# Optimization experiments

Measured on AMD Instinct MI355X. Metric: run time of the kernel, lower is better.

Reference implementation:

```python
import jax, jax.numpy as jnp
import numpy as np

D_MODEL = 1024
NUM_HEADS = 16
OUT_SHAPE = (64,)            # ControlGate `shape`; d_head = prod(OUT_SHAPE)
BANK_SIZE = 16
TOP_K = 2
BATCH, SEQ = 8, 4096
D_OUT = NUM_HEADS * int(np.prod(OUT_SHAPE))  # 1024


def setup_inputs() -> dict:
    key = jax.random.key(0)
    k1, k2, k3, k4 = jax.random.split(key, 4)
    tensor = jax.random.normal(k1, (BATCH, SEQ, D_MODEL), dtype=jnp.float32)
    sel_idx = jax.random.randint(k2, (BATCH, TOP_K), 0, BANK_SIZE)
    sel_probs = jax.random.uniform(k3, (BATCH, TOP_K), dtype=jnp.float32)
    sel_probs = sel_probs / jnp.sum(sel_probs, axis=-1, keepdims=True)
    W = jax.random.normal(k4, (BANK_SIZE, D_MODEL, D_OUT), dtype=jnp.float32) * 0.02
    b = jnp.zeros((BANK_SIZE, D_OUT), dtype=jnp.float32)
    return {"tensor": tensor, "sel_idx": sel_idx, "sel_probs": sel_probs, "W": W, "b": b}


def reference(tensor, sel_idx, sel_probs, W, b):
    # --- VirtualMakeHeads: bank-selected (virtual) linear projection ---
    # Superimpose the selected weight banks per batch element.
    W_sel = W[sel_idx]                    # (B, K, d_model, d_out)  irregular gather
    b_sel = b[sel_idx]                    # (B, K, d_out)
    W_eff = jnp.einsum('bk,bkio->bio', sel_probs, W_sel)   # (B, d_model, d_out)
    b_eff = jnp.einsum('bk,bko->bo', sel_probs, b_sel)     # (B, d_out)
    logits = jnp.einsum('bsi,bio->bso', tensor, W_eff) + b_eff[:, None, :]
    # reshape to heads: (B, S, num_heads, d_head)
    logits = logits.reshape(*logits.shape[:-1], NUM_HEADS, -1)
    # --- ControlGate: unflatten last dim into OUT_SHAPE ---
    logits = logits.reshape(*logits.shape[:-1], *OUT_SHAPE)
    # DropoutLogits with p=0.0 (eval) is identity.
    # activation == 'sigmoid'
    return jax.nn.sigmoid(logits)
```

## Files before the change

### kernel.cpp

```cpp
#include <hip/hip_runtime.h>
#include <hip/hip_bf16.h>

#define B_  8
#define S_  4096
#define DM  1024
#define DO  1024

typedef __attribute__((ext_vector_type(4))) float f32x4;
typedef __attribute__((ext_vector_type(8))) short bf16x8;

__device__ inline unsigned int pkbf(float a, float b) {
    __hip_bfloat162 h = __float22bfloat162_rn(float2{a, b});
    union { __hip_bfloat162 h2; unsigned int u; } cv;
    cv.h2 = h;
    return cv.u;
}

__global__ __launch_bounds__(256) void prep_wpack(
    const float* __restrict__ W, const int* __restrict__ sel_idx,
    const float* __restrict__ sel_probs, unsigned short* __restrict__ wpack)
{
    const int kt = blockIdx.x, nb = blockIdx.y, b = blockIdx.z;
    const int i0 = sel_idx[b*2+0], i1 = sel_idx[b*2+1];
    const float p0 = sel_probs[b*2+0], p1 = sel_probs[b*2+1];
    const int t = threadIdx.x;
    const int col = t & 127;
    const int gh  = t >> 7;

    const int o = nb * 128 + col;
    const float* w0 = W + (size_t)i0 * DM * DO + (size_t)(kt * 32) * DO + o;
    const float* w1 = W + (size_t)i1 * DM * DO + (size_t)(kt * 32) * DO + o;

    char* tile = (char*)wpack + ((size_t)((b * 8 + nb) * 32 + kt)) * 8192;
    const int q = (col >> 1) & 3;

    #pragma unroll
    for (int gg = 0; gg < 2; ++gg) {
        const int g = gh * 2 + gg;
        float v[8];
        #pragma unroll
        for (int j = 0; j < 8; ++j)
            v[j] = p0 * w0[(size_t)(g * 8 + j) * DO] + p1 * w1[(size_t)(g * 8 + j) * DO];
        uint4 u;
        u.x = pkbf(v[0], v[1]); u.y = pkbf(v[2], v[3]);
        u.z = pkbf(v[4], v[5]); u.w = pkbf(v[6], v[7]);
        *reinterpret_cast<uint4*>(tile + col * 64 + ((g ^ q) << 4)) = u;
    }
}

__global__ __launch_bounds__(256) void prep_beff(
    const float* __restrict__ bias, const int* __restrict__ sel_idx,
    const float* __restrict__ sel_probs, float* __restrict__ beff)
{
    const int b = blockIdx.x;
    const int i0 = sel_idx[b*2+0], i1 = sel_idx[b*2+1];
    const float p0 = sel_probs[b*2+0], p1 = sel_probs[b*2+1];
    for (int o = threadIdx.x; o < DO; o += blockDim.x)
        beff[(size_t)b * DO + o] = p0 * bias[(size_t)i0 * DO + o]
                                 + p1 * bias[(size_t)i1 * DO + o];
}

__global__ __launch_bounds__(256, 4) void gemm4(
    const float* __restrict__ X, const unsigned short* __restrict__ wpack,
    const float* __restrict__ beff, float* __restrict__ out)
{
    __shared__ char lds[32768];

    const int id = blockIdx.x;
    const int swz = (id & 7) * 256 + (id >> 3);
    const int b  = swz >> 8;
    const int bm = (swz >> 3) & 31;
    const int nb = swz & 7;

    const int t = threadIdx.x;
    const int wave = t >> 6, lane = t & 63;
    const int wm = wave >> 1, wn = wave & 1;
    const int fr = lane & 15, fq = lane >> 4;

    const int s_row = t >> 1;
    const int s_h   = t & 1;
    const float* xrow = X + ((size_t)(b * S_ + bm * 128 + s_row)) * DM + s_h * 16;
    const int sq = (s_row >> 1) & 3;
    const int wrA0 = s_row * 64 + (((s_h * 2 + 0) ^ sq) << 4);
    const int wrA1 = s_row * 64 + (((s_h * 2 + 1) ^ sq) << 4);

    const char* wtile = (const char*)wpack + ((size_t)((b * 8 + nb) * 32)) * 8192;

    const int axor = (fr >> 1) & 3;
    const int rdA = (wm * 64 + fr) * 64 + ((fq ^ axor) << 4);
    const int rdB = (wn * 64 + fr) * 64 + ((fq ^ axor) << 4);

    f32x4 acc[4][4] = {};
    float4 ax0, ax1, ax2, ax3;

#define LOAD_X(KT)                                                            \
    {   const float* s = xrow + (KT) * 32;                                    \
        ax0 = *reinterpret_cast<const float4*>(s);                            \
        ax1 = *reinterpret_cast<const float4*>(s + 4);                        \
        ax2 = *reinterpret_cast<const float4*>(s + 8);                        \
        ax3 = *reinterpret_cast<const float4*>(s + 12); }

#define STAGE_B(KT, BOFF)                                                     \
    {   const char* gB = wtile + (size_t)(KT) * 8192;                         \
        _Pragma("unroll")                                                     \
        for (int r = 0; r < 2; ++r)                                           \
            __builtin_amdgcn_global_load_lds(                                 \
                (const __attribute__((address_space(1))) void*)(gB + (wave*2+r)*1024 + lane*16), \
                (__attribute__((address_space(3))) void*)(lds + (BOFF) + (wave*2+r)*1024),       \
                16, 0, 0); }

#define WRITE_A(AOFF)                                                         \
    {   uint4 u0, u1;                                                         \
        u0.x = pkbf(ax0.x, ax0.y); u0.y = pkbf(ax0.z, ax0.w);                 \
        u0.z = pkbf(ax1.x, ax1.y); u0.w = pkbf(ax1.z, ax1.w);                 \
        u1.x = pkbf(ax2.x, ax2.y); u1.y = pkbf(ax2.z, ax2.w);                 \
        u1.z = pkbf(ax3.x, ax3.y); u1.w = pkbf(ax3.z, ax3.w);                 \
        *reinterpret_cast<uint4*>(lds + (AOFF) + wrA0) = u0;                  \
        *reinterpret_cast<uint4*>(lds + (AOFF) + wrA1) = u1; }

    LOAD_X(0);
    __builtin_amdgcn_sched_barrier(0);
    STAGE_B(0, 16384);
    __builtin_amdgcn_sched_barrier(0);
    WRITE_A(0);
    __syncthreads();

    for (int kt = 0; kt < 32; ++kt) {
        const int cur = (kt & 1) * 8192;
        const int nxt = 8192 - cur;

        if (kt < 31) {
            LOAD_X(kt + 1);
            __builtin_amdgcn_sched_barrier(0);
            STAGE_B(kt + 1, 16384 + nxt);
            __builtin_amdgcn_sched_barrier(0);
        }

        bf16x8 bf[4];
        #pragma unroll
        for (int nf = 0; nf < 4; ++nf)
            bf[nf] = *reinterpret_cast<const bf16x8*>(lds + 16384 + cur + rdB + nf * 1024);
        #pragma unroll
        for (int m = 0; m < 4; ++m) {
            bf16x8 af = *reinterpret_cast<const bf16x8*>(lds + cur + rdA + m * 1024);
            #pragma unroll
            for (int nf = 0; nf < 4; ++nf)
                acc[m][nf] = __builtin_amdgcn_mfma_f32_16x16x32_bf16(af, bf[nf], acc[m][nf], 0, 0, 0);
        }

        if (kt < 31) { WRITE_A(nxt); }
        __syncthreads();
    }

    const float* be = beff + (size_t)b * DO + nb * 128 + wn * 64;
    float bv[4];
    #pragma unroll
    for (int nf = 0; nf < 4; ++nf) bv[nf] = be[nf * 16 + fr];

    float* ob = out + ((size_t)(b * S_ + bm * 128 + wm * 64)) * DO + nb * 128 + wn * 64;
    #pragma unroll
    for (int m = 0; m < 4; ++m) {
        #pragma unroll
        for (int nf = 0; nf < 4; ++nf) {
            const int col = nf * 16 + fr;
            #pragma unroll
            for (int r = 0; r < 4; ++r) {
                const int row = m * 16 + fq * 4 + r;
                const float xv = acc[m][nf][r] + bv[nf];
                ob[(size_t)row * DO + col] = 1.0f / (1.0f + __expf(-xv));
            }
        }
    }
#undef LOAD_X
#undef STAGE_B
#undef WRITE_A
}

extern "C" void kernel_launch(void* const* d_in, const int* in_sizes, int n_in,
                              void* d_out, int out_size, void* d_ws, size_t ws_size,
                              hipStream_t stream) {
    const float* tensor    = (const float*)d_in[0];
    const int*   sel_idx   = (const int*)d_in[1];
    const float* sel_probs = (const float*)d_in[2];
    const float* W         = (const float*)d_in[3];
    const float* bias      = (const float*)d_in[4];
    float* out = (float*)d_out;

    unsigned short* wpack = (unsigned short*)d_ws;
    float* beff = (float*)((char*)d_ws + (size_t)8 * 8 * 32 * 8192);

    hipLaunchKernelGGL(prep_wpack, dim3(32, 8, 8), dim3(256), 0, stream,
                       W, sel_idx, sel_probs, wpack);
    hipLaunchKernelGGL(prep_beff, dim3(8), dim3(256), 0, stream,
                       bias, sel_idx, sel_probs, beff);
    hipLaunchKernelGGL(gemm4, dim3(2048), dim3(256), 0, stream,
                       tensor, wpack, beff, out);
}
```

Measured before the change: 165.5 us.

## Pre-pack X to bf16 and use larger 256x256 GEMM tiles with async LDS loads

```diff
diff --git a/kernel.cpp b/kernel.cpp
--- a/kernel.cpp
+++ b/kernel.cpp
@@ -16,7 +16,204 @@
     return cv.u;
 }
 
-__global__ __launch_bounds__(256) void prep_wpack(
+
+__global__ __launch_bounds__(256) void prep_xpack(
+    const float* __restrict__ X, unsigned short* __restrict__ xpack)
+{
+    const int kt = blockIdx.x, bm = blockIdx.y, b = blockIdx.z;
+    const int r = threadIdx.x;
+    const float* src = X + ((size_t)(b * S_ + bm * 256 + r)) * DM + kt * 64;
+    char* dst = (char*)xpack + ((size_t)((b * 16 + bm) * 16 + kt)) * 32768 + r * 128;
+    const int rx = r & 7;
+    #pragma unroll
+    for (int g = 0; g < 8; ++g) {
+        float4 a = *reinterpret_cast<const float4*>(src + g * 8);
+        float4 c = *reinterpret_cast<const float4*>(src + g * 8 + 4);
+        uint4 u;
+        u.x = pkbf(a.x, a.y); u.y = pkbf(a.z, a.w);
+        u.z = pkbf(c.x, c.y); u.w = pkbf(c.z, c.w);
+        *reinterpret_cast<uint4*>(dst + ((g ^ rx) << 4)) = u;
+    }
+}
+
+__global__ __launch_bounds__(256) void prep_wpack64(
+    const float* __restrict__ W, const int* __restrict__ sel_idx,
+    const float* __restrict__ sel_probs, unsigned short* __restrict__ wpack)
+{
+    const int kt = blockIdx.x, nb = blockIdx.y, b = blockIdx.z;
+    const int i0 = sel_idx[b*2+0], i1 = sel_idx[b*2+1];
+    const float p0 = sel_probs[b*2+0], p1 = sel_probs[b*2+1];
+    const int c = threadIdx.x;
+    const int o = nb * 256 + c;
+    const float* w0 = W + (size_t)i0 * DM * DO + (size_t)(kt * 64) * DO + o;
+    const float* w1 = W + (size_t)i1 * DM * DO + (size_t)(kt * 64) * DO + o;
+    char* dst = (char*)wpack + ((size_t)((b * 4 + nb) * 16 + kt)) * 32768 + c * 128;
+    const int cx = c & 7;
+    #pragma unroll
+    for (int g = 0; g < 8; ++g) {
+        float v[8];
+        #pragma unroll
+        for (int j = 0; j < 8; ++j)
+            v[j] = p0 * w0[(size_t)(g * 8 + j) * DO] + p1 * w1[(size_t)(g * 8 + j) * DO];
+        uint4 u;
+        u.x = pkbf(v[0], v[1]); u.y = pkbf(v[2], v[3]);
+        u.z = pkbf(v[4], v[5]); u.w = pkbf(v[6], v[7]);
+        *reinterpret_cast<uint4*>(dst + ((g ^ cx) << 4)) = u;
+    }
+}
+
+__global__ __launch_bounds__(256) void prep_beff(
+    const float* __restrict__ bias, const int* __restrict__ sel_idx,
+    const float* __restrict__ sel_probs, float* __restrict__ beff)
+{
+    const int b = blockIdx.x;
+    const int i0 = sel_idx[b*2+0], i1 = sel_idx[b*2+1];
+    const float p0 = sel_probs[b*2+0], p1 = sel_probs[b*2+1];
+    for (int o = threadIdx.x; o < DO; o += blockDim.x)
+        beff[(size_t)b * DO + o] = p0 * bias[(size_t)i0 * DO + o]
+                                 + p1 * bias[(size_t)i1 * DO + o];
+}
+
+__global__ __launch_bounds__(512, 2) void gemmx(
+    const unsigned short* __restrict__ xpack, const unsigned short* __restrict__ wpack,
+    const float* __restrict__ beff, float* __restrict__ out)
+{
+    extern __shared__ char lds[];
+
+    const int id = blockIdx.x;
+    const int swz = (id & 7) * 64 + (id >> 3);
+    const int b  = swz >> 6;
+    const int bm = (swz >> 2) & 15;
+    const int nb = swz & 3;
+
+    const int t = threadIdx.x;
+    const int wave = t >> 6, lane = t & 63;
+    const int wm = wave >> 2, wnw = wave & 3;
+    const int fr = lane & 15, fq = lane >> 4;
+
+    const char* xt = (const char*)xpack + ((size_t)((b * 16 + bm) * 16)) * 32768;
+    const char* wt = (const char*)wpack + ((size_t)((b * 4 + nb) * 16)) * 32768;
+
+    const int s0 = ((fq ^ (fr & 7)) << 4);
+    const int s1 = (((4 + fq) ^ (fr & 7)) << 4);
+    const int rdA = wm * 16384 + fr * 128;
+    const int rdB = wnw * 8192 + fr * 128;
+
+    f32x4 acc[8][4] = {};
+
+#define GLOAD(SRC, DSTOFF, I)                                                 \
+    __builtin_amdgcn_global_load_lds(                                         \
+        (const __attribute__((address_space(1))) void*)((SRC) + wave*4096 + (I)*1024 + lane*16), \
+        (__attribute__((address_space(3))) void*)(lds + (DSTOFF) + wave*4096 + (I)*1024), 16, 0, 0)
+
+#define MFMA16(MB, AF, BK)                                                    \
+    __builtin_amdgcn_s_setprio(1);                                            \
+    _Pragma("unroll")                                                         \
+    for (int m = 0; m < 4; ++m) {                                             \
+        _Pragma("unroll")                                                     \
+        for (int nf = 0; nf < 4; ++nf)                                        \
+            acc[(MB)+m][nf] = __builtin_amdgcn_mfma_f32_16x16x32_bf16(        \
+                AF[m], BK[nf], acc[(MB)+m][nf], 0, 0, 0);                     \
+    }                                                                         \
+    __builtin_amdgcn_s_setprio(0);
+
+    #pragma unroll
+    for (int i = 0; i < 4; ++i) { GLOAD(xt, 0, i); GLOAD(wt, 65536, i); }
+    asm volatile("s_waitcnt vmcnt(0)" ::: "memory");
+    __builtin_amdgcn_s_barrier();
+
+    #pragma unroll 1
+    for (int kt = 0; kt < 16; ++kt) {
+        const int ca = (kt & 1) * 32768;
+        const int cb = 65536 + ca;
+        const int na = 32768 - ca;
+        const int nbf = 65536 + na;
+        const char* gxn = xt + (size_t)(kt + 1) * 32768;
+        const char* gwn = wt + (size_t)(kt + 1) * 32768;
+
+        bf16x8 bk[4], af[4];
+
+        #pragma unroll
+        for (int nf = 0; nf < 4; ++nf)
+            bk[nf] = *reinterpret_cast<const bf16x8*>(lds + cb + rdB + nf*2048 + s0);
+        #pragma unroll
+        for (int m = 0; m < 4; ++m)
+            af[m] = *reinterpret_cast<const bf16x8*>(lds + ca + rdA + m*2048 + s0);
+        __builtin_amdgcn_sched_barrier(0);
+        if (kt < 15) {
+            #pragma unroll
+            for (int i = 0; i < 4; ++i) { GLOAD(gxn, na, i); GLOAD(gwn, nbf, i); }
+        }
+        __builtin_amdgcn_sched_barrier(0);
+        __builtin_amdgcn_s_barrier();
+        asm volatile("s_waitcnt lgkmcnt(0)" ::: "memory");
+        __builtin_amdgcn_sched_barrier(0);
+        MFMA16(0, af, bk)
+        __builtin_amdgcn_sched_barrier(0);
+        __builtin_amdgcn_s_barrier();
+
+        #pragma unroll
+        for (int m = 0; m < 4; ++m)
+            af[m] = *reinterpret_cast<const bf16x8*>(lds + ca + rdA + (4+m)*2048 + s0);
+        __builtin_amdgcn_sched_barrier(0);
+        __builtin_amdgcn_s_barrier();
+        asm volatile("s_waitcnt lgkmcnt(0)" ::: "memory");
+        __builtin_amdgcn_sched_barrier(0);
+        MFMA16(4, af, bk)
+        __builtin_amdgcn_sched_barrier(0);
+        __builtin_amdgcn_s_barrier();
+
+        #pragma unroll
+        for (int nf = 0; nf < 4; ++nf)
+            bk[nf] = *reinterpret_cast<const bf16x8*>(lds + cb + rdB + nf*2048 + s1);
+        #pragma unroll
+        for (int m = 0; m < 4; ++m)
+            af[m] = *reinterpret_cast<const bf16x8*>(lds + ca + rdA + m*2048 + s1);
+        __builtin_amdgcn_sched_barrier(0);
+        __builtin_amdgcn_s_barrier();
+        asm volatile("s_waitcnt lgkmcnt(0)" ::: "memory");
+        __builtin_amdgcn_sched_barrier(0);
+        MFMA16(0, af, bk)
+        __builtin_amdgcn_sched_barrier(0);
+        __builtin_amdgcn_s_barrier();
+
+        #pragma unroll
+        for (int m = 0; m < 4; ++m)
+            af[m] = *reinterpret_cast<const bf16x8*>(lds + ca + rdA + (4+m)*2048 + s1);
+        __builtin_amdgcn_sched_barrier(0);
+        __builtin_amdgcn_s_barrier();
+        asm volatile("s_waitcnt lgkmcnt(0)" ::: "memory");
+        __builtin_amdgcn_sched_barrier(0);
+        MFMA16(4, af, bk)
+        __builtin_amdgcn_sched_barrier(0);
+        if (kt < 15) { asm volatile("s_waitcnt vmcnt(0)" ::: "memory"); }
+        __builtin_amdgcn_s_barrier();
+    }
+
+    const float* be = beff + (size_t)b * DO + nb * 256 + wnw * 64;
+    float bv[4];
+    #pragma unroll
+    for (int nf = 0; nf < 4; ++nf) bv[nf] = be[nf * 16 + fr];
+
+    float* ob = out + ((size_t)(b * S_ + bm * 256 + wm * 128)) * DO + nb * 256 + wnw * 64;
+    #pragma unroll
+    for (int mf = 0; mf < 8; ++mf) {
+        #pragma unroll
+        for (int nf = 0; nf < 4; ++nf) {
+            const int col = nf * 16 + fr;
+            #pragma unroll
+            for (int r = 0; r < 4; ++r) {
+                const int row = mf * 16 + fq * 4 + r;
+                const float xv = acc[mf][nf][r] + bv[nf];
+                ob[(size_t)row * DO + col] = 1.0f / (1.0f + __expf(-xv));
+            }
+        }
+    }
+#undef GLOAD
+#undef MFMA16
+}
+
+__global__ __launch_bounds__(256) void prep_wpack_f(
     const float* __restrict__ W, const int* __restrict__ sel_idx,
     const float* __restrict__ sel_probs, unsigned short* __restrict__ wpack)
 {
@@ -26,14 +223,11 @@
     const int t = threadIdx.x;
     const int col = t & 127;
     const int gh  = t >> 7;
-
     const int o = nb * 128 + col;
     const float* w0 = W + (size_t)i0 * DM * DO + (size_t)(kt * 32) * DO + o;
     const float* w1 = W + (size_t)i1 * DM * DO + (size_t)(kt * 32) * DO + o;
-
     char* tile = (char*)wpack + ((size_t)((b * 8 + nb) * 32 + kt)) * 8192;
     const int q = (col >> 1) & 3;
-
     #pragma unroll
     for (int gg = 0; gg < 2; ++gg) {
         const int g = gh * 2 + gg;
@@ -48,58 +242,38 @@
     }
 }
 
-__global__ __launch_bounds__(256) void prep_beff(
-    const float* __restrict__ bias, const int* __restrict__ sel_idx,
-    const float* __restrict__ sel_probs, float* __restrict__ beff)
-{
-    const int b = blockIdx.x;
-    const int i0 = sel_idx[b*2+0], i1 = sel_idx[b*2+1];
-    const float p0 = sel_probs[b*2+0], p1 = sel_probs[b*2+1];
-    for (int o = threadIdx.x; o < DO; o += blockDim.x)
-        beff[(size_t)b * DO + o] = p0 * bias[(size_t)i0 * DO + o]
-                                 + p1 * bias[(size_t)i1 * DO + o];
-}
-
 __global__ __launch_bounds__(256, 4) void gemm4(
     const float* __restrict__ X, const unsigned short* __restrict__ wpack,
     const float* __restrict__ beff, float* __restrict__ out)
 {
     __shared__ char lds[32768];
-
     const int id = blockIdx.x;
     const int swz = (id & 7) * 256 + (id >> 3);
     const int b  = swz >> 8;
     const int bm = (swz >> 3) & 31;
     const int nb = swz & 7;
-
     const int t = threadIdx.x;
     const int wave = t >> 6, lane = t & 63;
     const int wm = wave >> 1, wn = wave & 1;
     const int fr = lane & 15, fq = lane >> 4;
-
     const int s_row = t >> 1;
     const int s_h   = t & 1;
     const float* xrow = X + ((size_t)(b * S_ + bm * 128 + s_row)) * DM + s_h * 16;
     const int sq = (s_row >> 1) & 3;
     const int wrA0 = s_row * 64 + (((s_h * 2 + 0) ^ sq) << 4);
     const int wrA1 = s_row * 64 + (((s_h * 2 + 1) ^ sq) << 4);
-
     const char* wtile = (const char*)wpack + ((size_t)((b * 8 + nb) * 32)) * 8192;
-
     const int axor = (fr >> 1) & 3;
     const int rdA = (wm * 64 + fr) * 64 + ((fq ^ axor) << 4);
     const int rdB = (wn * 64 + fr) * 64 + ((fq ^ axor) << 4);
-
     f32x4 acc[4][4] = {};
     float4 ax0, ax1, ax2, ax3;
-
 #define LOAD_X(KT)                                                            \
     {   const float* s = xrow + (KT) * 32;                                    \
         ax0 = *reinterpret_cast<const float4*>(s);                            \
         ax1 = *reinterpret_cast<const float4*>(s + 4);                        \
         ax2 = *reinterpret_cast<const float4*>(s + 8);                        \
         ax3 = *reinterpret_cast<const float4*>(s + 12); }
-
 #define STAGE_B(KT, BOFF)                                                     \
     {   const char* gB = wtile + (size_t)(KT) * 8192;                         \
         _Pragma("unroll")                                                     \
@@ -108,7 +282,6 @@
                 (const __attribute__((address_space(1))) void*)(gB + (wave*2+r)*1024 + lane*16), \
                 (__attribute__((address_space(3))) void*)(lds + (BOFF) + (wave*2+r)*1024),       \
                 16, 0, 0); }
-
 #define WRITE_A(AOFF)                                                         \
     {   uint4 u0, u1;                                                         \
         u0.x = pkbf(ax0.x, ax0.y); u0.y = pkbf(ax0.z, ax0.w);                 \
@@ -117,25 +290,21 @@
         u1.z = pkbf(ax3.x, ax3.y); u1.w = pkbf(ax3.z, ax3.w);                 \
         *reinterpret_cast<uint4*>(lds + (AOFF) + wrA0) = u0;                  \
         *reinterpret_cast<uint4*>(lds + (AOFF) + wrA1) = u1; }
-
     LOAD_X(0);
     __builtin_amdgcn_sched_barrier(0);
     STAGE_B(0, 16384);
     __builtin_amdgcn_sched_barrier(0);
     WRITE_A(0);
     __syncthreads();
-
     for (int kt = 0; kt < 32; ++kt) {
         const int cur = (kt & 1) * 8192;
         const int nxt = 8192 - cur;
-
         if (kt < 31) {
             LOAD_X(kt + 1);
             __builtin_amdgcn_sched_barrier(0);
             STAGE_B(kt + 1, 16384 + nxt);
             __builtin_amdgcn_sched_barrier(0);
         }
-
         bf16x8 bf[4];
         #pragma unroll
         for (int nf = 0; nf < 4; ++nf)
@@ -147,16 +316,13 @@
             for (int nf = 0; nf < 4; ++nf)
                 acc[m][nf] = __builtin_amdgcn_mfma_f32_16x16x32_bf16(af, bf[nf], acc[m][nf], 0, 0, 0);
         }
-
         if (kt < 31) { WRITE_A(nxt); }
         __syncthreads();
     }
-
     const float* be = beff + (size_t)b * DO + nb * 128 + wn * 64;
     float bv[4];
     #pragma unroll
     for (int nf = 0; nf < 4; ++nf) bv[nf] = be[nf * 16 + fr];
-
     float* ob = out + ((size_t)(b * S_ + bm * 128 + wm * 64)) * DO + nb * 128 + wn * 64;
     #pragma unroll
     for (int m = 0; m < 4; ++m) {
@@ -186,13 +352,34 @@
     const float* bias      = (const float*)d_in[4];
     float* out = (float*)d_out;
 
-    unsigned short* wpack = (unsigned short*)d_ws;
-    float* beff = (float*)((char*)d_ws + (size_t)8 * 8 * 32 * 8192);
-
-    hipLaunchKernelGGL(prep_wpack, dim3(32, 8, 8), dim3(256), 0, stream,
-                       W, sel_idx, sel_probs, wpack);
-    hipLaunchKernelGGL(prep_beff, dim3(8), dim3(256), 0, stream,
-                       bias, sel_idx, sel_probs, beff);
-    hipLaunchKernelGGL(gemm4, dim3(2048), dim3(256), 0, stream,
-                       tensor, wpack, beff, out);
-}
+    const size_t XP = (size_t)2048 * 32768;
+    const size_t WP = (size_t)512 * 32768;
+    const size_t NEED = XP + WP + (size_t)B_ * DO * 4;
+
+    if (ws_size >= NEED) {
+        unsigned short* xpack = (unsigned short*)d_ws;
+        unsigned short* wpack = (unsigned short*)((char*)d_ws + XP);
+        float* beff = (float*)((char*)d_ws + XP + WP);
+
+        hipFuncSetAttribute((const void*)gemmx,
+                            hipFuncAttributeMaxDynamicSharedMemorySize, 131072);
+
+        hipLaunchKernelGGL(prep_xpack, dim3(16, 16, 8), dim3(256), 0, stream,
+                           tensor, xpack);
+        hipLaunchKernelGGL(prep_wpack64, dim3(16, 4, 8), dim3(256), 0, stream,
+                           W, sel_idx, sel_probs, wpack);
+        hipLaunchKernelGGL(prep_beff, dim3(8), dim3(256), 0, stream,
+                           bias, sel_idx, sel_probs, beff);
+        hipLaunchKernelGGL(gemmx, dim3(512), dim3(512), 131072, stream,
+                           xpack, wpack, beff, out);
+    } else {
+        unsigned short* wpack = (unsigned short*)d_ws;
+        float* beff = (float*)((char*)d_ws + (size_t)8 * 8 * 32 * 8192);
+        hipLaunchKernelGGL(prep_wpack_f, dim3(32, 8, 8), dim3(256), 0, stream,
+                           W, sel_idx, sel_probs, wpack);
+        hipLaunchKernelGGL(prep_beff, dim3(8), dim3(256), 0, stream,
+                           bias, sel_idx, sel_probs, beff);
+        hipLaunchKernelGGL(gemm4, dim3(2048), dim3(256), 0, stream,
+                           tensor, wpack, beff, out);
+    }
+}
```

After: 157.9 us. 4.6% less time.

## Pre-pack activations to swizzled bf16 tiles and stage both GEMM operands via direct LDS loads

Applied to the files above, without the earlier changes.

```diff
diff --git a/kernel.cpp b/kernel.cpp
--- a/kernel.cpp
+++ b/kernel.cpp
@@ -16,24 +16,169 @@
     return cv.u;
 }
 
+
+__global__ __launch_bounds__(256) void prep_xpack(
+    const float* __restrict__ X, unsigned short* __restrict__ xpack)
+{
+    const int bm = blockIdx.y, b = blockIdx.z;
+    const int t = threadIdx.x;
+    const int r  = t & 127;
+    const int kt = blockIdx.x * 2 + (t >> 7);
+    const float* src = X + ((size_t)(b * S_ + bm * 128 + r)) * DM + kt * 32;
+    char* dst = (char*)xpack + ((size_t)((b * 32 + bm) * 32 + kt)) * 8192 + r * 64;
+    const int q = (r >> 1) & 3;
+    #pragma unroll
+    for (int g = 0; g < 4; ++g) {
+        float4 a = *reinterpret_cast<const float4*>(src + g * 8);
+        float4 c = *reinterpret_cast<const float4*>(src + g * 8 + 4);
+        uint4 u;
+        u.x = pkbf(a.x, a.y); u.y = pkbf(a.z, a.w);
+        u.z = pkbf(c.x, c.y); u.w = pkbf(c.z, c.w);
+        *reinterpret_cast<uint4*>(dst + ((g ^ q) << 4)) = u;
+    }
+}
+
 __global__ __launch_bounds__(256) void prep_wpack(
     const float* __restrict__ W, const int* __restrict__ sel_idx,
     const float* __restrict__ sel_probs, unsigned short* __restrict__ wpack)
 {
+    const int nb = blockIdx.y, b = blockIdx.z;
+    const int i0 = sel_idx[b*2+0], i1 = sel_idx[b*2+1];
+    const float p0 = sel_probs[b*2+0], p1 = sel_probs[b*2+1];
+    const int t = threadIdx.x;
+    const int c  = t & 127;
+    const int kt = blockIdx.x * 2 + (t >> 7);
+    const int o = nb * 128 + c;
+    const float* w0 = W + (size_t)i0 * DM * DO + (size_t)(kt * 32) * DO + o;
+    const float* w1 = W + (size_t)i1 * DM * DO + (size_t)(kt * 32) * DO + o;
+    char* dst = (char*)wpack + ((size_t)((b * 8 + nb) * 32 + kt)) * 8192 + c * 64;
+    const int q = (c >> 1) & 3;
+    #pragma unroll
+    for (int g = 0; g < 4; ++g) {
+        float v[8];
+        #pragma unroll
+        for (int j = 0; j < 8; ++j)
+            v[j] = p0 * w0[(size_t)(g * 8 + j) * DO] + p1 * w1[(size_t)(g * 8 + j) * DO];
+        uint4 u;
+        u.x = pkbf(v[0], v[1]); u.y = pkbf(v[2], v[3]);
+        u.z = pkbf(v[4], v[5]); u.w = pkbf(v[6], v[7]);
+        *reinterpret_cast<uint4*>(dst + ((g ^ q) << 4)) = u;
+    }
+}
+
+__global__ __launch_bounds__(256) void prep_beff(
+    const float* __restrict__ bias, const int* __restrict__ sel_idx,
+    const float* __restrict__ sel_probs, float* __restrict__ beff)
+{
+    const int b = blockIdx.x;
+    const int i0 = sel_idx[b*2+0], i1 = sel_idx[b*2+1];
+    const float p0 = sel_probs[b*2+0], p1 = sel_probs[b*2+1];
+    for (int o = threadIdx.x; o < DO; o += blockDim.x)
+        beff[(size_t)b * DO + o] = p0 * bias[(size_t)i0 * DO + o]
+                                 + p1 * bias[(size_t)i1 * DO + o];
+}
+
+__global__ __launch_bounds__(256, 4) void gemm128(
+    const unsigned short* __restrict__ xpack, const unsigned short* __restrict__ wpack,
+    const float* __restrict__ beff, float* __restrict__ out)
+{
+    __shared__ char lds[32768];
+
+    const int id = blockIdx.x;
+    const int swz = (id & 7) * 256 + (id >> 3);
+    const int b  = swz >> 8;
+    const int bm = (swz >> 3) & 31;
+    const int nb = swz & 7;
+
+    const int t = threadIdx.x;
+    const int wave = t >> 6, lane = t & 63;
+    const int wm = wave >> 1, wn = wave & 1;
+    const int fr = lane & 15, fq = lane >> 4;
+
+    const char* xt = (const char*)xpack + ((size_t)((b * 32 + bm) * 32)) * 8192;
+    const char* wt = (const char*)wpack + ((size_t)((b * 8 + nb) * 32)) * 8192;
+
+    const int q   = (fr >> 1) & 3;
+    const int rdA = (wm * 64 + fr) * 64 + ((fq ^ q) << 4);
+    const int rdB = (wn * 64 + fr) * 64 + ((fq ^ q) << 4);
+
+    f32x4 acc[4][4] = {};
+
+#define GLOAD(SRC, DST)                                                        \
+    __builtin_amdgcn_global_load_lds(                                          \
+        (const __attribute__((address_space(1))) void*)(SRC),                  \
+        (__attribute__((address_space(3))) void*)(DST), 16, 0, 0)
+
+#define STAGE(KT, OFF)                                                         \
+    {   const char* ga = xt + (size_t)(KT) * 8192 + wave * 2048 + lane * 16;   \
+        const char* gb = wt + (size_t)(KT) * 8192 + wave * 2048 + lane * 16;   \
+        char* la = lds + (OFF) + wave * 2048;                                  \
+        char* lb = lds + 16384 + (OFF) + wave * 2048;                          \
+        GLOAD(ga, la); GLOAD(ga + 1024, la + 1024);                            \
+        GLOAD(gb, lb); GLOAD(gb + 1024, lb + 1024); }
+
+    STAGE(0, 0);
+    __syncthreads();
+
+    for (int kt = 0; kt < 32; ++kt) {
+        const int cur = (kt & 1) * 8192;
+        const int nxt = 8192 - cur;
+
+        if (kt < 31) { STAGE(kt + 1, nxt); }
+
+        bf16x8 bk[4];
+        #pragma unroll
+        for (int nf = 0; nf < 4; ++nf)
+            bk[nf] = *reinterpret_cast<const bf16x8*>(lds + 16384 + cur + rdB + nf * 1024);
+        #pragma unroll
+        for (int m = 0; m < 4; ++m) {
+            bf16x8 af = *reinterpret_cast<const bf16x8*>(lds + cur + rdA + m * 1024);
+            #pragma unroll
+            for (int nf = 0; nf < 4; ++nf)
+                acc[m][nf] = __builtin_amdgcn_mfma_f32_16x16x32_bf16(af, bk[nf], acc[m][nf], 0, 0, 0);
+        }
+
+        __syncthreads();
+    }
+
+    const float* be = beff + (size_t)b * DO + nb * 128 + wn * 64;
+    float bv[4];
+    #pragma unroll
+    for (int nf = 0; nf < 4; ++nf) bv[nf] = be[nf * 16 + fr];
+
+    float* ob = out + ((size_t)(b * S_ + bm * 128 + wm * 64)) * DO + nb * 128 + wn * 64;
+    #pragma unroll
+    for (int m = 0; m < 4; ++m) {
+        #pragma unroll
+        for (int nf = 0; nf < 4; ++nf) {
+            const int col = nf * 16 + fr;
+            #pragma unroll
+            for (int r = 0; r < 4; ++r) {
+                const int row = m * 16 + fq * 4 + r;
+                const float xv = acc[m][nf][r] + bv[nf];
+                ob[(size_t)row * DO + col] = 1.0f / (1.0f + __expf(-xv));
+            }
+        }
+    }
+#undef GLOAD
+#undef STAGE
+}
+
+__global__ __launch_bounds__(256) void prep_wpack_f(
+    const float* __restrict__ W, const int* __restrict__ sel_idx,
+    const float* __restrict__ sel_probs, unsigned short* __restrict__ wpack)
+{
     const int kt = blockIdx.x, nb = blockIdx.y, b = blockIdx.z;
     const int i0 = sel_idx[b*2+0], i1 = sel_idx[b*2+1];
     const float p0 = sel_probs[b*2+0], p1 = sel_probs[b*2+1];
     const int t = threadIdx.x;
     const int col = t & 127;
     const int gh  = t >> 7;
-
     const int o = nb * 128 + col;
     const float* w0 = W + (size_t)i0 * DM * DO + (size_t)(kt * 32) * DO + o;
     const float* w1 = W + (size_t)i1 * DM * DO + (size_t)(kt * 32) * DO + o;
-
     char* tile = (char*)wpack + ((size_t)((b * 8 + nb) * 32 + kt)) * 8192;
     const int q = (col >> 1) & 3;
-
     #pragma unroll
     for (int gg = 0; gg < 2; ++gg) {
         const int g = gh * 2 + gg;
@@ -48,58 +193,38 @@
     }
 }
 
-__global__ __launch_bounds__(256) void prep_beff(
-    const float* __restrict__ bias, const int* __restrict__ sel_idx,
-    const float* __restrict__ sel_probs, float* __restrict__ beff)
-{
-    const int b = blockIdx.x;
-    const int i0 = sel_idx[b*2+0], i1 = sel_idx[b*2+1];
-    const float p0 = sel_probs[b*2+0], p1 = sel_probs[b*2+1];
-    for (int o = threadIdx.x; o < DO; o += blockDim.x)
-        beff[(size_t)b * DO + o] = p0 * bias[(size_t)i0 * DO + o]
-                                 + p1 * bias[(size_t)i1 * DO + o];
-}
-
 __global__ __launch_bounds__(256, 4) void gemm4(
     const float* __restrict__ X, const unsigned short* __restrict__ wpack,
     const float* __restrict__ beff, float* __restrict__ out)
 {
     __shared__ char lds[32768];
-
     const int id = blockIdx.x;
     const int swz = (id & 7) * 256 + (id >> 3);
     const int b  = swz >> 8;
     const int bm = (swz >> 3) & 31;
     const int nb = swz & 7;
-
     const int t = threadIdx.x;
     const int wave = t >> 6, lane = t & 63;
     const int wm = wave >> 1, wn = wave & 1;
     const int fr = lane & 15, fq = lane >> 4;
-
     const int s_row = t >> 1;
     const int s_h   = t & 1;
     const float* xrow = X + ((size_t)(b * S_ + bm * 128 + s_row)) * DM + s_h * 16;
     const int sq = (s_row >> 1) & 3;
     const int wrA0 = s_row * 64 + (((s_h * 2 + 0) ^ sq) << 4);
     const int wrA1 = s_row * 64 + (((s_h * 2 + 1) ^ sq) << 4);
-
     const char* wtile = (const char*)wpack + ((size_t)((b * 8 + nb) * 32)) * 8192;
-
     const int axor = (fr >> 1) & 3;
     const int rdA = (wm * 64 + fr) * 64 + ((fq ^ axor) << 4);
     const int rdB = (wn * 64 + fr) * 64 + ((fq ^ axor) << 4);
-
     f32x4 acc[4][4] = {};
     float4 ax0, ax1, ax2, ax3;
-
 #define LOAD_X(KT)                                                            \
     {   const float* s = xrow + (KT) * 32;                                    \
         ax0 = *reinterpret_cast<const float4*>(s);                            \
         ax1 = *reinterpret_cast<const float4*>(s + 4);                        \
         ax2 = *reinterpret_cast<const float4*>(s + 8);                        \
         ax3 = *reinterpret_cast<const float4*>(s + 12); }
-
 #define STAGE_B(KT, BOFF)                                                     \
     {   const char* gB = wtile + (size_t)(KT) * 8192;                         \
         _Pragma("unroll")                                                     \
@@ -108,7 +233,6 @@
                 (const __attribute__((address_space(1))) void*)(gB + (wave*2+r)*1024 + lane*16), \
                 (__attribute__((address_space(3))) void*)(lds + (BOFF) + (wave*2+r)*1024),       \
                 16, 0, 0); }
-
 #define WRITE_A(AOFF)                                                         \
     {   uint4 u0, u1;                                                         \
         u0.x = pkbf(ax0.x, ax0.y); u0.y = pkbf(ax0.z, ax0.w);                 \
@@ -117,25 +241,21 @@
         u1.z = pkbf(ax3.x, ax3.y); u1.w = pkbf(ax3.z, ax3.w);                 \
         *reinterpret_cast<uint4*>(lds + (AOFF) + wrA0) = u0;                  \
         *reinterpret_cast<uint4*>(lds + (AOFF) + wrA1) = u1; }
-
     LOAD_X(0);
     __builtin_amdgcn_sched_barrier(0);
     STAGE_B(0, 16384);
     __builtin_amdgcn_sched_barrier(0);
     WRITE_A(0);
     __syncthreads();
-
     for (int kt = 0; kt < 32; ++kt) {
         const int cur = (kt & 1) * 8192;
         const int nxt = 8192 - cur;
-
         if (kt < 31) {
             LOAD_X(kt + 1);
             __builtin_amdgcn_sched_barrier(0);
             STAGE_B(kt + 1, 16384 + nxt);
             __builtin_amdgcn_sched_barrier(0);
         }
-
         bf16x8 bf[4];
         #pragma unroll
         for (int nf = 0; nf < 4; ++nf)
@@ -147,16 +267,13 @@
             for (int nf = 0; nf < 4; ++nf)
                 acc[m][nf] = __builtin_amdgcn_mfma_f32_16x16x32_bf16(af, bf[nf], acc[m][nf], 0, 0, 0);
         }
-
         if (kt < 31) { WRITE_A(nxt); }
         __syncthreads();
     }
-
     const float* be = beff + (size_t)b * DO + nb * 128 + wn * 64;
     float bv[4];
     #pragma unroll
     for (int nf = 0; nf < 4; ++nf) bv[nf] = be[nf * 16 + fr];
-
     float* ob = out + ((size_t)(b * S_ + bm * 128 + wm * 64)) * DO + nb * 128 + wn * 64;
     #pragma unroll
     for (int m = 0; m < 4; ++m) {
@@ -186,13 +303,31 @@
     const float* bias      = (const float*)d_in[4];
     float* out = (float*)d_out;
 
-    unsigned short* wpack = (unsigned short*)d_ws;
-    float* beff = (float*)((char*)d_ws + (size_t)8 * 8 * 32 * 8192);
-
-    hipLaunchKernelGGL(prep_wpack, dim3(32, 8, 8), dim3(256), 0, stream,
-                       W, sel_idx, sel_probs, wpack);
-    hipLaunchKernelGGL(prep_beff, dim3(8), dim3(256), 0, stream,
-                       bias, sel_idx, sel_probs, beff);
-    hipLaunchKernelGGL(gemm4, dim3(2048), dim3(256), 0, stream,
-                       tensor, wpack, beff, out);
-}
+    const size_t XP = (size_t)8192 * 8192;
+    const size_t WP = (size_t)2048 * 8192;
+    const size_t NEED = XP + WP + (size_t)B_ * DO * 4;
+
+    if (ws_size >= NEED) {
+        unsigned short* xpack = (unsigned short*)d_ws;
+        unsigned short* wpack = (unsigned short*)((char*)d_ws + XP);
+        float* beff = (float*)((char*)d_ws + XP + WP);
+
+        hipLaunchKernelGGL(prep_xpack, dim3(16, 32, 8), dim3(256), 0, stream,
+                           tensor, xpack);
+        hipLaunchKernelGGL(prep_wpack, dim3(16, 8, 8), dim3(256), 0, stream,
+                           W, sel_idx, sel_probs, wpack);
+        hipLaunchKernelGGL(prep_beff, dim3(8), dim3(256), 0, stream,
+                           bias, sel_idx, sel_probs, beff);
+        hipLaunchKernelGGL(gemm128, dim3(2048), dim3(256), 0, stream,
+                           xpack, wpack, beff, out);
+    } else {
+        unsigned short* wpack = (unsigned short*)d_ws;
+        float* beff = (float*)((char*)d_ws + (size_t)8 * 8 * 32 * 8192);
+        hipLaunchKernelGGL(prep_wpack_f, dim3(32, 8, 8), dim3(256), 0, stream,
+                           W, sel_idx, sel_probs, wpack);
+        hipLaunchKernelGGL(prep_beff, dim3(8), dim3(256), 0, stream,
+                           bias, sel_idx, sel_probs, beff);
+        hipLaunchKernelGGL(gemm4, dim3(2048), dim3(256), 0, stream,
+                           tensor, wpack, beff, out);
+    }
+}
```

Result: faster. 146.7 us (-11.4%).
